# Kernel tuning notes

Measured on AMD Instinct MI355X. Metric: run time of the kernel, lower is better.

## Reference

```python
import jax, jax.numpy as jnp
import numpy as np

HEADS = 16
DIM_HEAD = 32
WSZ = 7
DIM = 512
INNER = HEADS * DIM_HEAD
LN_EPS = 1e-5


def setup_inputs() -> dict:
    key = jax.random.key(0)
    ks = jax.random.split(key, 9)
    b, H, W = 16, 56, 56
    x = jax.random.normal(ks[0], (b, DIM, H, W), dtype=jnp.float32)
    w_qkv = jax.random.normal(ks[1], (INNER * 3, DIM), dtype=jnp.float32) * (DIM ** -0.5)
    window_tokens = jax.random.normal(ks[2], (DIM,), dtype=jnp.float32)
    ln_w = jnp.ones((DIM_HEAD,), dtype=jnp.float32)
    ln_b = jnp.zeros((DIM_HEAD,), dtype=jnp.float32)
    w_qk = jax.random.normal(ks[3], (INNER * 2, INNER), dtype=jnp.float32) * (INNER ** -0.5)
    b_qk = jnp.zeros((INNER * 2,), dtype=jnp.float32)
    w_out = jax.random.normal(ks[4], (DIM, INNER), dtype=jnp.float32) * (INNER ** -0.5)
    b_out = jnp.zeros((DIM,), dtype=jnp.float32)
    return {"x": x, "w_qkv": w_qkv, "window_tokens": window_tokens,
            "ln_w": ln_w, "ln_b": ln_b, "w_qk": w_qk, "b_qk": b_qk,
            "w_out": w_out, "b_out": b_out}


def reference(x, w_qkv, window_tokens, ln_w, ln_b, w_qk, b_qk, w_out, b_out):
    b, c, H, W = x.shape
    h, d, wsz = HEADS, DIM_HEAD, WSZ
    X, Y = H // wsz, W // wsz
    nw = X * Y            # number of windows per image
    n = wsz * wsz         # tokens per window (49)
    scale = d ** -0.5

    # b c (X w1) (Y w2) -> (b X Y) c (w1 w2)
    xw = x.reshape(b, c, X, wsz, Y, wsz).transpose(0, 2, 4, 1, 3, 5).reshape(b * nw, c, n)
    wt = jnp.broadcast_to(window_tokens[None, :, None], (b * nw, c, 1))
    xc = jnp.concatenate([wt, xw], axis=-1)                 # [BW, c, n+1]

    qkv = jnp.einsum('oc,bcn->bon', w_qkv, xc)              # 1x1 conv, no bias
    q, k, v = jnp.split(qkv, 3, axis=1)
    def to_heads(t):
        return t.reshape(t.shape[0], h, d, n + 1).transpose(0, 1, 3, 2)  # [BW,h,n+1,d]
    q, k, v = to_heads(q), to_heads(k), to_heads(v)

    dots = jnp.einsum('bhid,bhjd->bhij', q * scale, k)      # [BW,h,50,50]
    attn = jax.nn.softmax(dots, axis=-1)
    out = jnp.einsum('bhij,bhjd->bhid', attn, v)            # [BW,h,50,d]

    wtok = out[:, :, 0].reshape(b, nw, h, d).transpose(0, 2, 1, 3)          # [b,h,nw,d]
    wfm = out[:, :, 1:].reshape(b, nw, h, n, d).transpose(0, 2, 1, 3, 4)    # [b,h,nw,n,d]

    # window_tokens_to_qk: LayerNorm(d) -> GELU -> conv1d(inner, 2*inner)
    mu = wtok.mean(-1, keepdims=True)
    var = wtok.var(-1, keepdims=True)
    normed = (wtok - mu) / jnp.sqrt(var + LN_EPS) * ln_w + ln_b
    g = jax.nn.gelu(normed, approximate=False)
    gf = g.transpose(0, 1, 3, 2).reshape(b, h * d, nw)      # b h n c -> b (h c) n
    qk = jnp.einsum('oc,bcn->bon', w_qk, gf) + b_qk[None, :, None]
    qk = qk.reshape(b, h, 2 * d, nw).transpose(0, 1, 3, 2)  # [b,h,nw,2d]
    w_q, w_k = qk[..., :d], qk[..., d:]

    w_dots = jnp.einsum('bhid,bhjd->bhij', w_q * scale, w_k)  # [b,h,nw,nw]
    w_attn = jax.nn.softmax(w_dots, axis=-1)
    agg = jnp.einsum('bhij,bhjnd->bhind', w_attn, wfm)        # [b,h,nw,n,d]

    # b h (X Y) (w1 w2) d -> b (h d) (X w1) (Y w2)
    fmap = agg.reshape(b, h, X, Y, wsz, wsz, d).transpose(0, 1, 6, 2, 4, 3, 5).reshape(b, h * d, H, W)
    return jnp.einsum('oc,bchw->bohw', w_out, fmap) + b_out[None, :, None, None]
```

## Files before the change

kernel.cpp:

```cpp
#include <hip/hip_runtime.h>
#include <math.h>

#define SCALE_D 0.17677669529663687f

typedef __attribute__((ext_vector_type(8))) short short8;
typedef __attribute__((ext_vector_type(4))) float f32x4;

__device__ __forceinline__ unsigned short f2bf(float f) {
  unsigned u = __builtin_bit_cast(unsigned, f);
  unsigned r = u + 0x7FFF + ((u >> 16) & 1);
  return (unsigned short)(r >> 16);
}
__device__ __forceinline__ float bf2f(unsigned short h) {
  unsigned u = ((unsigned)h) << 16;
  return __builtin_bit_cast(float, u);
}
__device__ __forceinline__ void gload16(const void* g, void* l) {
  __builtin_amdgcn_global_load_lds((const __attribute__((address_space(1))) unsigned int*)g,
                                   (__attribute__((address_space(3))) unsigned int*)l,
                                   16, 0, 0);
}

__global__ __launch_bounds__(256) void k_split(const float* __restrict__ src,
                                               unsigned short* __restrict__ hi,
                                               unsigned short* __restrict__ lo, int n) {
  int i = blockIdx.x * 256 + threadIdx.x;
  if (i < n) {
    float v = src[i];
    unsigned short h = f2bf(v);
    hi[i] = h;
    lo[i] = f2bf(v - bf2f(h));
  }
}

__global__ __launch_bounds__(256) void k_build_xcT(const float* __restrict__ x,
                                                   const float* __restrict__ wtok,
                                                   unsigned short* __restrict__ Thi,
                                                   unsigned short* __restrict__ Tlo,
                                                   int bb0) {
  const int cblk = blockIdx.x;
  const int h    = blockIdx.y;
  const int bbL  = blockIdx.z;
  const int bb   = bb0 + bbL;
  const int tid  = threadIdx.x;
  const int c0   = cblk * 64;
  if (h == 56) {
    for (int e = tid; e < 4096; e += 256) {
      int wl = e >> 6, cl = e & 63;
      float v = wtok[c0 + cl];
      unsigned short hv = f2bf(v);
      long idx = ((long)(bbL * 64 + wl) * 50) * 512 + c0 + cl;
      Thi[idx] = hv;
      Tlo[idx] = f2bf(v - bf2f(hv));
    }
    return;
  }
  __shared__ unsigned short shi[64][57], slo[64][57];
  const int Xw = h / 7, r7 = h % 7;
  for (int e = tid; e < 3584; e += 256) {
    int cl = e / 56, w = e - cl * 56;
    float v = x[((long)(bb * 512 + c0 + cl) * 56 + h) * 56 + w];
    unsigned short hv = f2bf(v);
    shi[cl][w] = hv;
    slo[cl][w] = f2bf(v - bf2f(hv));
  }
  __syncthreads();
  for (int e = tid; e < 3584; e += 256) {
    int row = e >> 6, cl = e & 63;
    int Yw = row / 7, c7 = row - Yw * 7;
    long trow = (long)(bbL * 64 + Xw * 8 + Yw) * 50 + 1 + r7 * 7 + c7;
    Thi[trow * 512 + c0 + cl] = shi[cl][row];
    Tlo[trow * 512 + c0 + cl] = slo[cl][row];
  }
}

template <int PACK>
__global__ __launch_bounds__(256, 2) void k_gemm_mfma(
    const unsigned short* __restrict__ Ahi, const unsigned short* __restrict__ Alo,
    const unsigned short* __restrict__ Bhi, const unsigned short* __restrict__ Blo,
    float* __restrict__ C, const float* __restrict__ bias,
    int NC, int brow_stride, long c_stride) {
  __shared__ unsigned short lds[2][4][128][32];
  const int tid = threadIdx.x;
  const int wv = tid >> 6, lane = tid & 63;

  const int gy = gridDim.y;
  const int nwg = gridDim.x * gy;
  int hw = blockIdx.y * gridDim.x + blockIdx.x;
  int flat;
  {
    int q = nwg >> 3, r = nwg & 7;
    int xcd = hw & 7, k = hw >> 3;
    int start = (xcd < r) ? xcd * (q + 1) : r * (q + 1) + (xcd - r) * q;
    flat = start + k;
  }
  const int bx = flat / gy, by = flat % gy;
  const int m0 = by * 128, n0 = bx * 128;
  const long brow0 = (long)blockIdx.z * brow_stride + n0;
  C += (long)blockIdx.z * c_stride;

  const int wr = wv >> 1, wc = wv & 1;
  const int lr = lane & 15, kb = lane >> 4;
  const int srow = lane >> 2, sju = lane & 3;
  const int sswz = (sju ^ ((srow >> 1) & 3)) * 8;
  const int rswz = (lr >> 1) & 3;

  f32x4 acc[4][4];
#pragma unroll
  for (int i = 0; i < 4; ++i)
#pragma unroll
    for (int j = 0; j < 4; ++j) {
      f32x4 z = {0.f, 0.f, 0.f, 0.f};
      acc[i][j] = z;
    }

  auto STAGE = [&](int buf, int k0) {
#pragma unroll
    for (int it = 0; it < 2; ++it) {
      const int rloc = (wv * 2 + it) * 16;
      const int r = rloc + srow;
      const long ga = (long)(m0 + r) * 512 + k0 + sswz;
      gload16(Ahi + ga, &lds[buf][0][rloc][0]);
      gload16(Alo + ga, &lds[buf][1][rloc][0]);
      const long gb = (brow0 + r) * 512 + k0 + sswz;
      gload16(Bhi + gb, &lds[buf][2][rloc][0]);
      gload16(Blo + gb, &lds[buf][3][rloc][0]);
    }
  };

  STAGE(0, 0);
  int cur = 0;
  for (int t = 0; t < 16; ++t) {
    if (t < 15) STAGE(cur ^ 1, (t + 1) * 32);
    if (t < 15) {
      asm volatile("s_waitcnt vmcnt(8)" ::: "memory");
    } else {
      asm volatile("s_waitcnt vmcnt(0)" ::: "memory");
    }
    __builtin_amdgcn_s_barrier();
    asm volatile("" ::: "memory");
    short8 ah[4], al[4], bh[4], bl[4];
#pragma unroll
    for (int f = 0; f < 4; ++f) {
      int ra = wr * 64 + f * 16 + lr;
      int ca = (kb ^ rswz) * 8;
      ah[f] = *(const short8*)&lds[cur][0][ra][ca];
      al[f] = *(const short8*)&lds[cur][1][ra][ca];
      int rb = wc * 64 + f * 16 + lr;
      bh[f] = *(const short8*)&lds[cur][2][rb][ca];
      bl[f] = *(const short8*)&lds[cur][3][rb][ca];
    }
#pragma unroll
    for (int i = 0; i < 4; ++i)
#pragma unroll
      for (int j = 0; j < 4; ++j) {
        acc[i][j] = __builtin_amdgcn_mfma_f32_16x16x32_bf16(ah[i], bh[j], acc[i][j], 0, 0, 0);
        acc[i][j] = __builtin_amdgcn_mfma_f32_16x16x32_bf16(ah[i], bl[j], acc[i][j], 0, 0, 0);
        acc[i][j] = __builtin_amdgcn_mfma_f32_16x16x32_bf16(al[i], bh[j], acc[i][j], 0, 0, 0);
      }
    asm volatile("s_waitcnt lgkmcnt(0)" ::: "memory");
    __builtin_amdgcn_s_barrier();
    asm volatile("" ::: "memory");
    cur ^= 1;
  }

#pragma unroll
  for (int i = 0; i < 4; ++i)
#pragma unroll
    for (int nf = 0; nf < 4; ++nf) {
      int col = n0 + wc * 64 + nf * 16 + lr;
      if (col < NC) {
#pragma unroll
        for (int j4 = 0; j4 < 4; ++j4) {
          int row = m0 + wr * 64 + i * 16 + kb * 4 + j4;
          float v = acc[i][nf][j4];
          if (PACK) {
            unsigned short h = f2bf(v);
            unsigned short l = f2bf(v - bf2f(h));
            ((unsigned*)C)[(long)row * NC + col] = (unsigned)h | ((unsigned)l << 16);
          } else {
            C[(long)row * NC + col] = v + (bias ? bias[row] : 0.f);
          }
        }
      }
    }
}

__global__ __launch_bounds__(256) void k_attn1_mfma(const unsigned* __restrict__ QKV,
                                                    float* __restrict__ OUT1, int w0) {
  __shared__ unsigned short P[4][16][72];
  const int tid = threadIdx.x;
  const int wv = tid >> 6, lane = tid & 63;
  const int idx = blockIdx.x * 4 + wv;
  const int wl = idx >> 4, h = idx & 15;
  const int lr = lane & 15, kb = lane >> 4;
  const long tb = (long)wl * 50;

  short8 kh[4], kl[4];
#pragma unroll
  for (int jt = 0; jt < 4; ++jt) {
#pragma unroll
    for (int e = 0; e < 8; ++e) {
      unsigned u = QKV[(long)(512 + h * 32 + kb * 8 + e) * 12800 + tb + jt * 16 + lr];
      kh[jt][e] = (short)(u & 0xFFFF);
      kl[jt][e] = (short)(u >> 16);
    }
  }
  short8 vh[2][2], vl[2][2];
#pragma unroll
  for (int ddt = 0; ddt < 2; ++ddt)
#pragma unroll
    for (int ks = 0; ks < 2; ++ks) {
      const long vb = (long)(1024 + h * 32 + ddt * 16 + lr) * 12800 + tb + ks * 32 + kb * 8;
#pragma unroll
      for (int e = 0; e < 8; ++e) {
        int j = ks * 32 + kb * 8 + e;
        unsigned u = (j < 50) ? QKV[vb + e] : 0u;
        vh[ddt][ks][e] = (short)(u & 0xFFFF);
        vl[ddt][ks][e] = (short)(u >> 16);
      }
    }

  const long ob = (long)((w0 + wl) * 16 + h) * 1600;

  for (int it = 0; it < 4; ++it) {
    short8 qh, ql;
#pragma unroll
    for (int e = 0; e < 8; ++e) {
      unsigned u = QKV[(long)(h * 32 + kb * 8 + e) * 12800 + tb + it * 16 + lr];
      qh[e] = (short)(u & 0xFFFF);
      ql[e] = (short)(u >> 16);
    }
    f32x4 s[4];
#pragma unroll
    for (int jt = 0; jt < 4; ++jt) {
      f32x4 z = {0.f, 0.f, 0.f, 0.f};
      s[jt] = z;
      s[jt] = __builtin_amdgcn_mfma_f32_16x16x32_bf16(qh, kh[jt], s[jt], 0, 0, 0);
      s[jt] = __builtin_amdgcn_mfma_f32_16x16x32_bf16(qh, kl[jt], s[jt], 0, 0, 0);
      s[jt] = __builtin_amdgcn_mfma_f32_16x16x32_bf16(ql, kh[jt], s[jt], 0, 0, 0);
#pragma unroll
      for (int r = 0; r < 4; ++r) s[jt][r] *= SCALE_D;
    }
    if (lr >= 2) {
#pragma unroll
      for (int r = 0; r < 4; ++r) s[3][r] = -1e30f;
    }
    float ex[4][4], rinv[4];
#pragma unroll
    for (int r = 0; r < 4; ++r) {
      float m = fmaxf(fmaxf(s[0][r], s[1][r]), fmaxf(s[2][r], s[3][r]));
      m = fmaxf(m, __shfl_xor(m, 1));
      m = fmaxf(m, __shfl_xor(m, 2));
      m = fmaxf(m, __shfl_xor(m, 4));
      m = fmaxf(m, __shfl_xor(m, 8));
      float sm = 0.f;
#pragma unroll
      for (int jt = 0; jt < 4; ++jt) {
        ex[jt][r] = __expf(s[jt][r] - m);
        sm += ex[jt][r];
      }
      sm += __shfl_xor(sm, 1);
      sm += __shfl_xor(sm, 2);
      sm += __shfl_xor(sm, 4);
      sm += __shfl_xor(sm, 8);
      rinv[r] = 1.f / sm;
    }
#pragma unroll
    for (int jt = 0; jt < 4; ++jt)
#pragma unroll
      for (int r = 0; r < 4; ++r)
        P[wv][kb * 4 + r][jt * 16 + lr] = f2bf(ex[jt][r] * rinv[r]);
    short8 pa0 = *(const short8*)&P[wv][lr][kb * 8];
    short8 pa1 = *(const short8*)&P[wv][lr][32 + kb * 8];
    f32x4 o[2];
#pragma unroll
    for (int ddt = 0; ddt < 2; ++ddt) {
      f32x4 z = {0.f, 0.f, 0.f, 0.f};
      o[ddt] = z;
      o[ddt] = __builtin_amdgcn_mfma_f32_16x16x32_bf16(pa0, vh[ddt][0], o[ddt], 0, 0, 0);
      o[ddt] = __builtin_amdgcn_mfma_f32_16x16x32_bf16(pa0, vl[ddt][0], o[ddt], 0, 0, 0);
      o[ddt] = __builtin_amdgcn_mfma_f32_16x16x32_bf16(pa1, vh[ddt][1], o[ddt], 0, 0, 0);
      o[ddt] = __builtin_amdgcn_mfma_f32_16x16x32_bf16(pa1, vl[ddt][1], o[ddt], 0, 0, 0);
    }
#pragma unroll
    for (int ddt = 0; ddt < 2; ++ddt)
#pragma unroll
      for (int r = 0; r < 4; ++r) {
        int i = it * 16 + kb * 4 + r;
        if (i < 50) OUT1[ob + i * 32 + ddt * 16 + lr] = o[ddt][r];
      }
  }
}

__global__ __launch_bounds__(256) void k_gemm(const float* __restrict__ A,
                                              const float* __restrict__ Bg,
                                              float* __restrict__ C,
                                              const float* __restrict__ bias,
                                              int M, int N, int K, long sB, long sC) {
  Bg += (long)blockIdx.z * sB;
  C  += (long)blockIdx.z * sC;
  __shared__ __align__(16) float As[32][132];
  __shared__ __align__(16) float Bs[32][132];
  const int tid = threadIdx.x;
  const int tx = tid & 15, ty = tid >> 4;
  const int m0 = blockIdx.y * 128, n0 = blockIdx.x * 128;

  float acc[8][8];
#pragma unroll
  for (int q = 0; q < 8; ++q)
#pragma unroll
    for (int r = 0; r < 8; ++r) acc[q][r] = 0.f;

  for (int k0 = 0; k0 < K; k0 += 32) {
#pragma unroll
    for (int it = 0; it < 4; ++it) {
      int idx = tid + it * 256;
      int row = idx >> 3, c4 = idx & 7;
      const float4 f = *(const float4*)&A[(long)(m0 + row) * K + k0 + c4 * 4];
      As[c4 * 4 + 0][row] = f.x;
      As[c4 * 4 + 1][row] = f.y;
      As[c4 * 4 + 2][row] = f.z;
      As[c4 * 4 + 3][row] = f.w;
    }
#pragma unroll
    for (int it = 0; it < 4; ++it) {
      int idx = tid + it * 256;
      int row = idx >> 5, c4 = idx & 31;
      int col = n0 + c4 * 4;
      float4 f;
      if (col + 3 < N) {
        f = *(const float4*)&Bg[(long)(k0 + row) * N + col];
      } else {
        f.x = (col + 0 < N) ? Bg[(long)(k0 + row) * N + col + 0] : 0.f;
        f.y = (col + 1 < N) ? Bg[(long)(k0 + row) * N + col + 1] : 0.f;
        f.z = (col + 2 < N) ? Bg[(long)(k0 + row) * N + col + 2] : 0.f;
        f.w = (col + 3 < N) ? Bg[(long)(k0 + row) * N + col + 3] : 0.f;
      }
      *(float4*)&Bs[row][c4 * 4] = f;
    }
    __syncthreads();
#pragma unroll
    for (int kk = 0; kk < 32; ++kk) {
      const float4 a0 = *(const float4*)&As[kk][ty * 8];
      const float4 a1 = *(const float4*)&As[kk][ty * 8 + 4];
      const float4 b0 = *(const float4*)&Bs[kk][tx * 8];
      const float4 b1 = *(const float4*)&Bs[kk][tx * 8 + 4];
      const float am[8] = {a0.x, a0.y, a0.z, a0.w, a1.x, a1.y, a1.z, a1.w};
      const float bn[8] = {b0.x, b0.y, b0.z, b0.w, b1.x, b1.y, b1.z, b1.w};
#pragma unroll
      for (int q = 0; q < 8; ++q)
#pragma unroll
        for (int r = 0; r < 8; ++r) acc[q][r] += am[q] * bn[r];
    }
    __syncthreads();
  }

#pragma unroll
  for (int q = 0; q < 8; ++q) {
    int m = m0 + ty * 8 + q;
    float bv = bias ? bias[m] : 0.f;
#pragma unroll
    for (int half = 0; half < 8; half += 4) {
      int col = n0 + tx * 8 + half;
#pragma unroll
      for (int rr = 0; rr < 4; ++rr)
        if (col + rr < N) C[(long)m * N + col + rr] = acc[q][half + rr] + bv;
    }
  }
}

__global__ __launch_bounds__(256) void k_ln_gelu(const float* __restrict__ OUT1,
                                                 const float* __restrict__ lnw,
                                                 const float* __restrict__ lnb,
                                                 float* __restrict__ G) {
  const int tid = threadIdx.x;
  const int r = blockIdx.x * 8 + (tid >> 5);
  const int l = tid & 31;
  const int bb = r >> 10, hh = (r >> 6) & 15, wp = r & 63;
  float v = OUT1[((long)((bb * 64 + wp) * 16 + hh)) * 1600 + l];
  float s = v, s2 = v * v;
#pragma unroll
  for (int o = 16; o >= 1; o >>= 1) {
    s += __shfl_xor(s, o, 32);
    s2 += __shfl_xor(s2, o, 32);
  }
  float mu = s * (1.f / 32.f);
  float var = s2 * (1.f / 32.f) - mu * mu;
  float xn = (v - mu) * rsqrtf(var + 1e-5f) * lnw[l] + lnb[l];
  float g = 0.5f * xn * (1.f + erff(xn * 0.70710678118654752f));
  G[((long)(bb * 512 + hh * 32 + l)) * 64 + wp] = g;
}

__global__ __launch_bounds__(256) void k_attn2_mfma(const float* __restrict__ QK,
                                                    const float* __restrict__ OUT1,
                                                    float* __restrict__ AGG) {
  const int bh = blockIdx.x;
  const int bb = bh >> 4, hh = bh & 15;
  const int tid = threadIdx.x;
  const int wv = tid >> 6, lane = tid & 63;
  const int lr = lane & 15, kb = lane >> 4;
  const int wr = wv >> 1, wc = wv & 1;

  __shared__ float wqs[64 * 33], wks[64 * 33];
  __shared__ float sd[64 * 65];
  __shared__ float smx[64], ssum[64];
  __shared__ __align__(16) unsigned short PAh[64][72], PAl[64][72];
  __shared__ __align__(16) unsigned short VTh[64][72], VTl[64][72];

  for (int t = tid; t < 2048; t += 256) {
    int dd = t >> 6, i = t & 63;
    wqs[i * 33 + dd] = QK[((long)(bb * 1024 + hh * 64 + dd)) * 64 + i] * SCALE_D;
    wks[i * 33 + dd] = QK[((long)(bb * 1024 + hh * 64 + 32 + dd)) * 64 + i];
  }
  __syncthreads();
  for (int t = tid; t < 4096; t += 256) {
    int i = t >> 6, j = t & 63;
    float s = 0.f;
#pragma unroll
    for (int dd = 0; dd < 32; ++dd) s += wqs[i * 33 + dd] * wks[j * 33 + dd];
    sd[i * 65 + j] = s;
  }
  __syncthreads();
  if (tid < 64) {
    float mx = -1e30f;
    for (int j = 0; j < 64; ++j) mx = fmaxf(mx, sd[tid * 65 + j]);
    float sm = 0.f;
    for (int j = 0; j < 64; ++j) sm += expf(sd[tid * 65 + j] - mx);
    smx[tid] = mx;
    ssum[tid] = 1.f / sm;
  }
  __syncthreads();
  for (int t = tid; t < 4096; t += 256) {
    int i = t >> 6, j = t & 63;
    float p = expf(sd[i * 65 + j] - smx[i]) * ssum[i];
    unsigned short h = f2bf(p);
    PAh[i][j] = h;
    PAl[i][j] = f2bf(p - bf2f(h));
  }
  __syncthreads();

  const int jstart = blockIdx.y * 13;
  const int ntiles = (blockIdx.y == 0) ? 13 : 12;
  const int swp = tid >> 2, sq = tid & 3;
  const long vbase = ((long)((bb * 64 + swp) * 16 + hh)) * 1600 + 32;
  const long abase = (long)bh * 100352;

  for (int tt = 0; tt < ntiles; ++tt) {
    const int jt = jstart + tt;
    const int jd0 = jt * 64;
    const int JT = (jt == 24) ? 32 : 64;
    for (int jj = 0; jj < (JT >> 4); ++jj) {
      const float4 v4 = *(const float4*)&OUT1[vbase + jd0 + jj * 16 + sq * 4];
#pragma unroll
      for (int e = 0; e < 4; ++e) {
        int jl = jj * 16 + sq * 4 + e;
        float v = (e == 0) ? v4.x : (e == 1) ? v4.y : (e == 2) ? v4.z : v4.w;
        unsigned short h = f2bf(v);
        VTh[jl][swp] = h;
        VTl[jl][swp] = f2bf(v - bf2f(h));
      }
    }
    __syncthreads();
#pragma unroll
    for (int mt = 0; mt < 2; ++mt) {
      const int i0 = wr * 32 + mt * 16;
#pragma unroll
      for (int nt = 0; nt < 2; ++nt) {
        const int jl0 = wc * 32 + nt * 16;
        if (jl0 < JT) {
          f32x4 acc = {0.f, 0.f, 0.f, 0.f};
#pragma unroll
          for (int ks = 0; ks < 2; ++ks) {
            const short8 pah = *(const short8*)&PAh[i0 + lr][ks * 32 + kb * 8];
            const short8 pal = *(const short8*)&PAl[i0 + lr][ks * 32 + kb * 8];
            const short8 vth = *(const short8*)&VTh[jl0 + lr][ks * 32 + kb * 8];
            const short8 vtl = *(const short8*)&VTl[jl0 + lr][ks * 32 + kb * 8];
            acc = __builtin_amdgcn_mfma_f32_16x16x32_bf16(pah, vth, acc, 0, 0, 0);
            acc = __builtin_amdgcn_mfma_f32_16x16x32_bf16(pah, vtl, acc, 0, 0, 0);
            acc = __builtin_amdgcn_mfma_f32_16x16x32_bf16(pal, vth, acc, 0, 0, 0);
          }
#pragma unroll
          for (int r = 0; r < 4; ++r)
            AGG[abase + (long)(i0 + kb * 4 + r) * 1568 + jd0 + jl0 + lr] = acc[r];
        }
      }
    }
    __syncthreads();
  }
}

__global__ __launch_bounds__(256) void k_fmap_T(const float* __restrict__ AGG,
                                                unsigned short* __restrict__ Thi,
                                                unsigned short* __restrict__ Tlo) {
  const int wp = blockIdx.x, bb = blockIdx.y;
  const int Xw = wp >> 3, Yw = wp & 7;
  const int c = threadIdx.x * 2;
  const int hh = c >> 5, d0 = c & 31;
  const long abase = ((long)(bb * 16 + hh) * 64 + wp) * 1568;
  for (int j = 0; j < 49; ++j) {
    float v0 = AGG[abase + j * 32 + d0];
    float v1 = AGG[abase + j * 32 + d0 + 1];
    int hw = (Xw * 7 + j / 7) * 56 + Yw * 7 + j % 7;
    long t = ((long)bb * 3200 + hw) * 512 + c;
    unsigned short h0 = f2bf(v0), h1 = f2bf(v1);
    unsigned short l0 = f2bf(v0 - bf2f(h0)), l1 = f2bf(v1 - bf2f(h1));
    *(unsigned*)&Thi[t] = (unsigned)h0 | ((unsigned)h1 << 16);
    *(unsigned*)&Tlo[t] = (unsigned)l0 | ((unsigned)l1 << 16);
  }
}

__global__ __launch_bounds__(256) void k_padzero(unsigned short* __restrict__ Thi,
                                                 unsigned short* __restrict__ Tlo) {
  const int bb = blockIdx.x;
  for (int e = threadIdx.x; e < 32768; e += 256) {
    long idx = ((long)bb * 3200 + 3136) * 512 + e;
    Thi[idx] = 0;
    Tlo[idx] = 0;
  }
}

extern "C" void kernel_launch(void* const* d_in, const int* in_sizes, int n_in,
                              void* d_out, int out_size, void* d_ws, size_t ws_size,
                              hipStream_t stream) {
  const float* x     = (const float*)d_in[0];
  const float* w_qkv = (const float*)d_in[1];
  const float* wt    = (const float*)d_in[2];
  const float* lnw   = (const float*)d_in[3];
  const float* lnb   = (const float*)d_in[4];
  const float* w_qk  = (const float*)d_in[5];
  const float* b_qk  = (const float*)d_in[6];
  const float* w_out = (const float*)d_in[7];
  const float* b_out = (const float*)d_in[8];
  float* out = (float*)d_out;
  float* ws  = (float*)d_ws;

  float* OUT1 = ws;
  float* AUX  = ws + 26214400L;
  unsigned short* XThi = (unsigned short*)(ws + 21233664L);
  unsigned short* XTlo = XThi + 6553600L;
  float* G  = AUX;
  float* QK = AUX + 524288L;
  unsigned short* WOhi = (unsigned short*)AUX;
  unsigned short* WOlo = WOhi + 262144L;
  unsigned short* FThi = (unsigned short*)ws;
  unsigned short* FTlo = FThi + 26214400L;

  unsigned* QKVc = (unsigned*)d_out;
  unsigned short* Whi = (unsigned short*)(out + 19660800L);
  unsigned short* Wlo = Whi + 786432L;
  float* AGG = out;

  k_split<<<3072, 256, 0, stream>>>(w_qkv, Whi, Wlo, 786432);
  for (int c = 0; c < 4; ++c) {
    k_build_xcT<<<dim3(8, 57, 4), 256, 0, stream>>>(x, wt, XThi, XTlo, c * 4);
    k_gemm_mfma<1><<<dim3(100, 12, 1), 256, 0, stream>>>(Whi, Wlo, XThi, XTlo,
                                                         (float*)QKVc, nullptr,
                                                         12800, 0, 0);
    k_attn1_mfma<<<1024, 256, 0, stream>>>(QKVc, OUT1, c * 256);
  }
  k_ln_gelu<<<2048, 256, 0, stream>>>(OUT1, lnw, lnb, G);
  k_gemm<<<dim3(1, 8, 16), 256, 0, stream>>>(w_qk, G, QK, b_qk,
                                             1024, 64, 512, 512L * 64, 1024L * 64);
  k_split<<<1024, 256, 0, stream>>>(w_out, WOhi, WOlo, 262144);
  k_attn2_mfma<<<dim3(256, 2, 1), 256, 0, stream>>>(QK, OUT1, AGG);
  k_fmap_T<<<dim3(64, 16), 256, 0, stream>>>(AGG, FThi, FTlo);
  k_padzero<<<16, 256, 0, stream>>>(FThi, FTlo);
  k_gemm_mfma<0><<<dim3(25, 4, 16), 256, 0, stream>>>(WOhi, WOlo, FThi, FTlo, out,
                                                      b_out, 3136, 3200, 512L * 3136);
}
```

Baseline: 788.9 us.

## Load A fragments directly from global and halve LDS to raise GEMM occupancy

The GEMM kernel no longer stages the A (hi/lo) tiles through LDS. Each wave reads its A fragments straight from global memory into registers, and only B is double-buffered in LDS. LDS use per block drops by half and launch bounds rise to 4 blocks per CU, aiming at higher occupancy and fewer LDS reads. The cost is redundant, uncoalesced global loads of A across waves that share rows (the two wc waves), plus extra register pressure under the tighter bound. Those global A loads are also now exposed in the loop without prefetch.

After: 921.9 us. +16.9%, slower.

```diff
diff --git a/kernel.cpp b/kernel.cpp
--- a/kernel.cpp
+++ b/kernel.cpp
@@ -75,12 +75,12 @@
 }
 
 template <int PACK>
-__global__ __launch_bounds__(256, 2) void k_gemm_mfma(
+__global__ __launch_bounds__(256, 4) void k_gemm_mfma(
     const unsigned short* __restrict__ Ahi, const unsigned short* __restrict__ Alo,
     const unsigned short* __restrict__ Bhi, const unsigned short* __restrict__ Blo,
     float* __restrict__ C, const float* __restrict__ bias,
     int NC, int brow_stride, long c_stride) {
-  __shared__ unsigned short lds[2][4][128][32];
+  __shared__ unsigned short lds[2][2][128][32];
   const int tid = threadIdx.x;
   const int wv = tid >> 6, lane = tid & 63;
 
@@ -103,7 +103,8 @@
   const int lr = lane & 15, kb = lane >> 4;
   const int srow = lane >> 2, sju = lane & 3;
   const int sswz = (sju ^ ((srow >> 1) & 3)) * 8;
-  const int rswz = (lr >> 1) & 3;
+  const int ca = (kb ^ ((lr >> 1) & 3)) * 8;
+  const long arow = (long)(m0 + wr * 64 + lr) * 512 + kb * 8;
 
   f32x4 acc[4][4];
 #pragma unroll
@@ -114,50 +115,47 @@
       acc[i][j] = z;
     }
 
-  auto STAGE = [&](int buf, int k0) {
+  auto STAGE_B = [&](int buf, int k0) {
 #pragma unroll
     for (int it = 0; it < 2; ++it) {
-      const int rloc = (wv * 2 + it) * 16;
-      const int r = rloc + srow;
-      const long ga = (long)(m0 + r) * 512 + k0 + sswz;
-      gload16(Ahi + ga, &lds[buf][0][rloc][0]);
-      gload16(Alo + ga, &lds[buf][1][rloc][0]);
-      const long gb = (brow0 + r) * 512 + k0 + sswz;
-      gload16(Bhi + gb, &lds[buf][2][rloc][0]);
-      gload16(Blo + gb, &lds[buf][3][rloc][0]);
+      const int rloc = wv * 32 + it * 16;
+      const long gb = (brow0 + rloc + srow) * 512 + k0 + sswz;
+      gload16(Bhi + gb, &lds[buf][0][rloc][0]);
+      gload16(Blo + gb, &lds[buf][1][rloc][0]);
     }
   };
 
-  STAGE(0, 0);
+  STAGE_B(0, 0);
   int cur = 0;
   for (int t = 0; t < 16; ++t) {
-    if (t < 15) STAGE(cur ^ 1, (t + 1) * 32);
+    const int k0 = t * 32;
+    short8 ah[4], al[4];
+#pragma unroll
+    for (int f = 0; f < 4; ++f) {
+      const long ga = arow + (long)f * 16 * 512 + k0;
+      ah[f] = *(const short8*)&Ahi[ga];
+      al[f] = *(const short8*)&Alo[ga];
+    }
     if (t < 15) {
-      asm volatile("s_waitcnt vmcnt(8)" ::: "memory");
+      STAGE_B(cur ^ 1, k0 + 32);
+      asm volatile("s_waitcnt vmcnt(4)" ::: "memory");
     } else {
       asm volatile("s_waitcnt vmcnt(0)" ::: "memory");
     }
     __builtin_amdgcn_s_barrier();
     asm volatile("" ::: "memory");
-    short8 ah[4], al[4], bh[4], bl[4];
-#pragma unroll
-    for (int f = 0; f < 4; ++f) {
-      int ra = wr * 64 + f * 16 + lr;
-      int ca = (kb ^ rswz) * 8;
-      ah[f] = *(const short8*)&lds[cur][0][ra][ca];
-      al[f] = *(const short8*)&lds[cur][1][ra][ca];
-      int rb = wc * 64 + f * 16 + lr;
-      bh[f] = *(const short8*)&lds[cur][2][rb][ca];
-      bl[f] = *(const short8*)&lds[cur][3][rb][ca];
-    }
-#pragma unroll
-    for (int i = 0; i < 4; ++i)
-#pragma unroll
-      for (int j = 0; j < 4; ++j) {
-        acc[i][j] = __builtin_amdgcn_mfma_f32_16x16x32_bf16(ah[i], bh[j], acc[i][j], 0, 0, 0);
-        acc[i][j] = __builtin_amdgcn_mfma_f32_16x16x32_bf16(ah[i], bl[j], acc[i][j], 0, 0, 0);
-        acc[i][j] = __builtin_amdgcn_mfma_f32_16x16x32_bf16(al[i], bh[j], acc[i][j], 0, 0, 0);
-      }
+#pragma unroll
+    for (int j = 0; j < 4; ++j) {
+      int rb = wc * 64 + j * 16 + lr;
+      const short8 bh = *(const short8*)&lds[cur][0][rb][ca];
+      const short8 bl = *(const short8*)&lds[cur][1][rb][ca];
+#pragma unroll
+      for (int i = 0; i < 4; ++i) {
+        acc[i][j] = __builtin_amdgcn_mfma_f32_16x16x32_bf16(ah[i], bh, acc[i][j], 0, 0, 0);
+        acc[i][j] = __builtin_amdgcn_mfma_f32_16x16x32_bf16(ah[i], bl, acc[i][j], 0, 0, 0);
+        acc[i][j] = __builtin_amdgcn_mfma_f32_16x16x32_bf16(al[i], bh, acc[i][j], 0, 0, 0);
+      }
+    }
     asm volatile("s_waitcnt lgkmcnt(0)" ::: "memory");
     __builtin_amdgcn_s_barrier();
     asm volatile("" ::: "memory");
```
